# Optimization experiments

Measured on AMD Instinct MI355X. Metric: run time of the kernel, lower is better.

The kernel has to match this reference:

```python
import jax, jax.numpy as jnp
import numpy as np

N, M, D = 6144, 6144, 128
EPS = 1e-12


def setup_inputs() -> dict:
    key = jax.random.key(0)
    k1, k2 = jax.random.split(key)
    desc1 = jax.random.normal(k1, (N, D), dtype=jnp.float32)
    desc2 = jax.random.normal(k2, (M, D), dtype=jnp.float32)
    # DISK descriptors are unit-normalized; distances in the docstring are in [0, 2]
    desc1 = desc1 / jnp.linalg.norm(desc1, axis=-1, keepdims=True)
    desc2 = desc2 / jnp.linalg.norm(desc2, axis=-1, keepdims=True)
    inverse_T = jnp.asarray(15.0, dtype=jnp.float32)  # learned scalar nn.Parameter
    return {"desc1": desc1, "desc2": desc2, "inverse_T": inverse_T}


def reference(desc1, desc2, inverse_T):
    # pairwise Euclidean distance matrix [N, M]
    sq1 = jnp.sum(desc1 * desc1, axis=-1)            # [N]
    sq2 = jnp.sum(desc2 * desc2, axis=-1)            # [M]
    inner = desc1 @ desc2.T                           # [N, M] GEMM, D=128
    d2 = sq1[:, None] + sq2[None, :] - 2.0 * inner
    distances = jnp.sqrt(jnp.maximum(d2, 0.0) + EPS)  # [N, M]

    affinity = -inverse_T * distances                 # scaled logits

    # Categorical(logits=affinity).logits  == log_softmax over rows
    # Categorical(logits=affinity.T).logits.T == log_softmax over columns
    logp_I = jax.nn.log_softmax(affinity, axis=1)     # row distribution [N, M]
    logp_T = jax.nn.log_softmax(affinity, axis=0)     # col distribution [N, M]

    dense_logp = logp_I + logp_T                      # dual-softmax log prob
    dense_p = jnp.exp(logp_I) * jnp.exp(logp_T)       # dual-softmax prob

    # mle(): argmax matches with cycle-consistency check
    maxes_I = jnp.argmax(affinity, axis=1)            # [N] best col per row
    maxes_T = jnp.argmax(affinity, axis=0)            # [M] best row per col
    idx = jnp.arange(N)
    cycle_consistent = maxes_T[maxes_I] == idx        # [N] bool mask
    # Original returns stack([right[paired_left], paired_left]) over the
    # consistent subset; here we keep fixed shape [2, N] + the mask
    # (matches[:, i] valid iff cycle_consistent[i]).
    matches = jnp.stack([idx, maxes_I], axis=0)       # [2, N] int

    return dense_logp, dense_p, matches, cycle_consistent
```

## Files before the change

kernel.cpp:

```cpp
#include <hip/hip_runtime.h>
#include <hip/hip_bf16.h>
#include <stdint.h>

#define NROWS 6144
#define MCOLS 6144
#define DDIM  128
#define EPSQ  1e-12f
#define NTC   48

typedef unsigned long long ull;
typedef __attribute__((ext_vector_type(8))) short short8;
typedef __attribute__((ext_vector_type(4))) float floatx4;

__device__ __forceinline__ ull makeKey(float v, int idx) {
    unsigned u = __float_as_uint(v);
    u = (u & 0x80000000u) ? ~u : (u | 0x80000000u);
    return ((ull)u << 32) | (ull)(0xFFFFFFFFu - (unsigned)idx);
}
__device__ __forceinline__ int decodeKeyIdx(ull k) {
    return (int)(0xFFFFFFFFu - (unsigned)(k & 0xFFFFFFFFull));
}
__device__ __forceinline__ unsigned short f2bf(float f) {
    unsigned u = __float_as_uint(f);
    u += 0x7fffu + ((u >> 16) & 1);
    return (unsigned short)(u >> 16);
}

#define DPPF(x, ctrl) __uint_as_float(__builtin_amdgcn_update_dpp( \
    0, (int)__float_as_uint(x), (ctrl), 0xF, 0xF, false))
#define DPPI(x, ctrl) __builtin_amdgcn_update_dpp(0, (x), (ctrl), 0xF, 0xF, false)
#define ROR8 0x128
#define ROR4 0x124
#define ROR2 0x122
#define ROR1 0x121

#define GLOAD16(g, l) \
  __builtin_amdgcn_global_load_lds((const __attribute__((address_space(1))) unsigned int*)(g), \
                                   (__attribute__((address_space(3))) unsigned int*)(l), 16, 0, 0)

__device__ __forceinline__ void tileCoord(int& rowBase, int& colBase) {
    int id  = blockIdx.x;
    int wid = (id & 7) * (NTC * NTC / 8) + (id >> 3);
    rowBase = (wid / NTC) * 128;
    colBase = (wid % NTC) * 128;
}

__global__ __launch_bounds__(256) void convert_kernel(
    const float* __restrict__ d1, const float* __restrict__ d2,
    unsigned short* __restrict__ s1, unsigned short* __restrict__ s2,
    float* __restrict__ sq1, float* __restrict__ sq2,
    unsigned* __restrict__ zero_region)
{
    int tid = blockIdx.x * 256 + threadIdx.x;
    if (tid < 36864) zero_region[tid] = 0u;

    int row = tid >> 4;
    int sub = tid & 15;
    if (row >= NROWS + MCOLS) return;
    bool isA = row < NROWS;
    int r = isA ? row : row - NROWS;
    const float* src = (isA ? d1 : d2) + (size_t)r * DDIM + sub * 8;
    unsigned short* dst = (isA ? s1 : s2) + (size_t)r * 256;

    float4 v0 = *(const float4*)(src);
    float4 v1 = *(const float4*)(src + 4);
    float vs[8] = {v0.x, v0.y, v0.z, v0.w, v1.x, v1.y, v1.z, v1.w};

    float s = 0.f;
    #pragma unroll
    for (int j = 0; j < 8; ++j) s += vs[j] * vs[j];
    #pragma unroll
    for (int m = 1; m < 16; m <<= 1) s += __shfl_xor(s, m, 64);
    if (sub == 0) { if (isA) sq1[r] = s; else sq2[r] = s; }

    short8 hi, lo;
    #pragma unroll
    for (int j = 0; j < 8; ++j) {
        unsigned short h = f2bf(vs[j]);
        hi[j] = (short)h;
        lo[j] = (short)f2bf(vs[j] - __uint_as_float((unsigned)h << 16));
    }
    int e  = sub * 8;
    int c  = e >> 6;
    int pe = (e & 63) ^ ((r & 7) << 3);
    *(short8*)(dst + c * 128 + pe)      = hi;
    *(short8*)(dst + c * 128 + 64 + pe) = lo;
}

__device__ __forceinline__ void stageBuf(
    const unsigned short* __restrict__ gpanel, unsigned short* buf,
    int c, int h, int t)
{
    #pragma unroll
    for (int it = 0; it < 2; ++it) {
        int li = t * 8 + it * 4096;
        int r  = li >> 6, e = li & 63;
        int gi = r * 256 + c * 128 + h * 64 + e;
        GLOAD16(gpanel + gi, &buf[li]);
    }
}

__device__ __forceinline__ void computeChunk3(
    const unsigned short* Ah_, const unsigned short* Al_,
    const unsigned short* Bh_, const unsigned short* Bl_,
    int lane, int wr, int wc, floatx4 acc[4][2])
{
    const int l15 = lane & 15;
    const int q16 = (lane >> 4) * 16;
    const int sw  = (l15 & 7) << 4;
    const char* Ah = (const char*)Ah_;
    const char* Al = (const char*)Al_;
    const char* Bh = (const char*)Bh_;
    const char* Bl = (const char*)Bl_;
    #pragma unroll
    for (int ks = 0; ks < 2; ++ks) {
        const int kk = (ks * 64 + q16) ^ sw;
        short8 afh[4], afl[4], bfh[2], bfl[2];
        #pragma unroll
        for (int mi = 0; mi < 4; ++mi) {
            afh[mi] = *(const short8*)(Ah + (wr * 64 + mi * 16 + l15) * 128 + kk);
            afl[mi] = *(const short8*)(Al + (wr * 64 + mi * 16 + l15) * 128 + kk);
        }
        #pragma unroll
        for (int ni = 0; ni < 2; ++ni) {
            bfh[ni] = *(const short8*)(Bh + (wc * 32 + ni * 16 + l15) * 128 + kk);
            bfl[ni] = *(const short8*)(Bl + (wc * 32 + ni * 16 + l15) * 128 + kk);
        }
        #pragma unroll
        for (int mi = 0; mi < 4; ++mi)
            #pragma unroll
            for (int ni = 0; ni < 2; ++ni)
                acc[mi][ni] = __builtin_amdgcn_mfma_f32_16x16x32_bf16(
                    bfh[ni], afh[mi], acc[mi][ni], 0, 0, 0);
        #pragma unroll
        for (int mi = 0; mi < 4; ++mi)
            #pragma unroll
            for (int ni = 0; ni < 2; ++ni)
                acc[mi][ni] = __builtin_amdgcn_mfma_f32_16x16x32_bf16(
                    bfl[ni], afh[mi], acc[mi][ni], 0, 0, 0);
        #pragma unroll
        for (int mi = 0; mi < 4; ++mi)
            #pragma unroll
            for (int ni = 0; ni < 2; ++ni)
                acc[mi][ni] = __builtin_amdgcn_mfma_f32_16x16x32_bf16(
                    bfh[ni], afl[mi], acc[mi][ni], 0, 0, 0);
    }
}

__device__ __forceinline__ void computeChunk2(
    const unsigned short* Ah_, const unsigned short* Al_,
    const unsigned short* Bh_,
    int lane, int wr, int wc, floatx4 acc[4][2])
{
    const int l15 = lane & 15;
    const int q16 = (lane >> 4) * 16;
    const int sw  = (l15 & 7) << 4;
    const char* Ah = (const char*)Ah_;
    const char* Al = (const char*)Al_;
    const char* Bh = (const char*)Bh_;
    #pragma unroll
    for (int ks = 0; ks < 2; ++ks) {
        const int kk = (ks * 64 + q16) ^ sw;
        short8 afh[4], afl[4], bfh[2];
        #pragma unroll
        for (int mi = 0; mi < 4; ++mi) {
            afh[mi] = *(const short8*)(Ah + (wr * 64 + mi * 16 + l15) * 128 + kk);
            afl[mi] = *(const short8*)(Al + (wr * 64 + mi * 16 + l15) * 128 + kk);
        }
        #pragma unroll
        for (int ni = 0; ni < 2; ++ni)
            bfh[ni] = *(const short8*)(Bh + (wc * 32 + ni * 16 + l15) * 128 + kk);
        #pragma unroll
        for (int mi = 0; mi < 4; ++mi)
            #pragma unroll
            for (int ni = 0; ni < 2; ++ni)
                acc[mi][ni] = __builtin_amdgcn_mfma_f32_16x16x32_bf16(
                    bfh[ni], afh[mi], acc[mi][ni], 0, 0, 0);
        #pragma unroll
        for (int mi = 0; mi < 4; ++mi)
            #pragma unroll
            for (int ni = 0; ni < 2; ++ni)
                acc[mi][ni] = __builtin_amdgcn_mfma_f32_16x16x32_bf16(
                    bfh[ni], afl[mi], acc[mi][ni], 0, 0, 0);
    }
}

__global__ __launch_bounds__(512, 4) void gemm_reduce_kernel(
    const unsigned short* __restrict__ s1, const unsigned short* __restrict__ s2,
    const float* __restrict__ invT,
    const float* __restrict__ sq1, const float* __restrict__ sq2,
    float* __restrict__ rowsum, float* __restrict__ colsum,
    ull* __restrict__ rowkey, ull* __restrict__ colkey)
{
    __shared__ unsigned short A0[8192], A1[8192], B0[8192], B1[8192];
    __shared__ float lRowS[128], lColS[128];
    __shared__ ull   lRowK[128], lColK[128];

    const int t = threadIdx.x;
    const int lane = t & 63;
    const int wave = t >> 6;
    const int wr = wave >> 2, wc = wave & 3;
    int rowBase, colBase;
    tileCoord(rowBase, colBase);
    const unsigned short* gA = s1 + (size_t)rowBase * 256;
    const unsigned short* gB = s2 + (size_t)colBase * 256;

    if (t < 128) { lRowS[t] = 0.f; lColS[t] = 0.f; lRowK[t] = 0ull; lColK[t] = 0ull; }

    floatx4 acc[4][2] = {};
    stageBuf(gA, A0, 0, 0, t); stageBuf(gA, A1, 0, 1, t);
    stageBuf(gB, B0, 0, 0, t); stageBuf(gB, B1, 0, 1, t);
    __syncthreads();
    computeChunk3(A0, A1, B0, B1, lane, wr, wc, acc);
    __syncthreads();
    stageBuf(gA, A0, 1, 0, t); stageBuf(gA, A1, 1, 1, t);
    stageBuf(gB, B0, 1, 0, t); stageBuf(gB, B1, 1, 1, t);
    __syncthreads();
    computeChunk3(A0, A1, B0, B1, lane, wr, wc, acc);

    const int l15 = lane & 15;
    const int q   = lane >> 4;
    const float iT = *invT;
    float s1r[4];
    #pragma unroll
    for (int mi = 0; mi < 4; ++mi)
        s1r[mi] = sq1[rowBase + wr * 64 + mi * 16 + l15] + EPSQ;
    const int colLoc0 = wc * 32 + q * 4;
    float4 s2v[2];
    #pragma unroll
    for (int ni = 0; ni < 2; ++ni)
        s2v[ni] = *(const float4*)(sq2 + colBase + colLoc0 + ni * 16);

    float rs[4], rv[4]; int rj[4];
    float cs[2][4], cv[2][4]; int ci[2][4];
    #pragma unroll
    for (int ni = 0; ni < 2; ++ni)
        #pragma unroll
        for (int r = 0; r < 4; ++r) { cs[ni][r] = 0.f; cv[ni][r] = -1e30f; ci[ni][r] = 0; }

    #pragma unroll
    for (int mi = 0; mi < 4; ++mi) {
        const int gi = rowBase + wr * 64 + mi * 16 + l15;
        rs[mi] = 0.f; rv[mi] = -1e30f; rj[mi] = 0;
        #pragma unroll
        for (int ni = 0; ni < 2; ++ni) {
            #pragma unroll
            for (int r = 0; r < 4; ++r) {
                float sv2 = (r == 0) ? s2v[ni].x : (r == 1) ? s2v[ni].y
                          : (r == 2) ? s2v[ni].z : s2v[ni].w;
                float dd = s1r[mi] + sv2 - 2.0f * acc[mi][ni][r];
                float v = -iT * __builtin_amdgcn_sqrtf(fmaxf(dd, EPSQ));
                float e = __expf(v);
                rs[mi] += e;
                if (v > rv[mi]) { rv[mi] = v; rj[mi] = colBase + colLoc0 + ni * 16 + r; }
                cs[ni][r] += e;
                if (v > cv[ni][r]) { cv[ni][r] = v; ci[ni][r] = gi; }
            }
        }
    }

    #pragma unroll
    for (int mi = 0; mi < 4; ++mi) {
        float s = rs[mi];
        s += __shfl_xor(s, 16, 64); s += __shfl_xor(s, 32, 64);
        float v = rv[mi];
        v = fmaxf(v, __shfl_xor(v, 16, 64)); v = fmaxf(v, __shfl_xor(v, 32, 64));
        int cand = (rv[mi] == v) ? rj[mi] : 0x7FFFFFFF;
        cand = min(cand, __shfl_xor(cand, 16, 64));
        cand = min(cand, __shfl_xor(cand, 32, 64));
        if (lane < 16) {
            int idx = wr * 64 + mi * 16 + l15;
            atomicAdd(&lRowS[idx], s);
            atomicMax(&lRowK[idx], makeKey(v, cand));
        }
    }

    #pragma unroll
    for (int ni = 0; ni < 2; ++ni)
        #pragma unroll
        for (int r = 0; r < 4; ++r) {
            float s = cs[ni][r];
            s += DPPF(s, ROR8); s += DPPF(s, ROR4); s += DPPF(s, ROR2); s += DPPF(s, ROR1);
            float v = cv[ni][r];
            v = fmaxf(v, DPPF(v, ROR8)); v = fmaxf(v, DPPF(v, ROR4));
            v = fmaxf(v, DPPF(v, ROR2)); v = fmaxf(v, DPPF(v, ROR1));
            int cand = (cv[ni][r] == v) ? ci[ni][r] : 0x7FFFFFFF;
            cand = min(cand, DPPI(cand, ROR8)); cand = min(cand, DPPI(cand, ROR4));
            cand = min(cand, DPPI(cand, ROR2)); cand = min(cand, DPPI(cand, ROR1));
            if (l15 == 0) {
                int idx = colLoc0 + ni * 16 + r;
                atomicAdd(&lColS[idx], s);
                atomicMax(&lColK[idx], makeKey(v, cand));
            }
        }
    __syncthreads();

    if (t < 128) {
        atomicAdd(&rowsum[rowBase + t], lRowS[t]);
        atomicMax(&rowkey[rowBase + t], lRowK[t]);
    } else if (t < 256) {
        int j = t - 128;
        atomicAdd(&colsum[colBase + j], lColS[j]);
        atomicMax(&colkey[colBase + j], lColK[j]);
    }
}

#define VSTRIDE 132
__global__ __launch_bounds__(512, 4) void gemm_write_kernel(
    const unsigned short* __restrict__ s1, const unsigned short* __restrict__ s2,
    const float* __restrict__ invT,
    const float* __restrict__ sq1, const float* __restrict__ sq2,
    const float* __restrict__ rowsum, const float* __restrict__ colsum,
    const ull* __restrict__ rowkey, const ull* __restrict__ colkey,
    float* __restrict__ logp_out, float* __restrict__ p_out,
    float* __restrict__ out_matches, float* __restrict__ out_cyc)
{
    __shared__ char SMEM[128 * VSTRIDE * 4];
    unsigned short* A0 = (unsigned short*)(SMEM);
    unsigned short* A1 = (unsigned short*)(SMEM + 16384);
    unsigned short* B0 = (unsigned short*)(SMEM + 32768);
    unsigned short* B1 = (unsigned short*)(SMEM + 49152);
    float* V = (float*)SMEM;

    const int t = threadIdx.x;
    const int lane = t & 63;
    const int wave = t >> 6;
    const int wr = wave >> 2, wc = wave & 3;
    int rowBase, colBase;
    tileCoord(rowBase, colBase);
    const unsigned short* gA = s1 + (size_t)rowBase * 256;
    const unsigned short* gB = s2 + (size_t)colBase * 256;

    if (colBase == 0 && t < 128) {
        int i = rowBase + t;
        int mi = decodeKeyIdx(rowkey[i]);
        out_matches[i]         = (float)i;
        out_matches[NROWS + i] = (float)mi;
        out_cyc[i] = (decodeKeyIdx(colkey[mi]) == i) ? 1.0f : 0.0f;
    }

    floatx4 acc[4][2] = {};
    stageBuf(gA, A0, 0, 0, t); stageBuf(gA, A1, 0, 1, t);
    stageBuf(gB, B0, 0, 0, t); stageBuf(gB, B1, 1, 0, t);
    __syncthreads();
    computeChunk2(A0, A1, B0, lane, wr, wc, acc);
    __syncthreads();
    stageBuf(gA, A0, 1, 0, t); stageBuf(gA, A1, 1, 1, t);
    __syncthreads();
    computeChunk2(A0, A1, B1, lane, wr, wc, acc);

    const int l15 = lane & 15;
    const int q   = lane >> 4;
    const float iT = *invT;
    float s1r[4];
    #pragma unroll
    for (int mi = 0; mi < 4; ++mi)
        s1r[mi] = sq1[rowBase + wr * 64 + mi * 16 + l15] + EPSQ;
    const int colLoc0 = wc * 32 + q * 4;
    float4 s2v[2];
    #pragma unroll
    for (int ni = 0; ni < 2; ++ni)
        s2v[ni] = *(const float4*)(sq2 + colBase + colLoc0 + ni * 16);

    __syncthreads();
    #pragma unroll
    for (int mi = 0; mi < 4; ++mi) {
        const int lrow = wr * 64 + mi * 16 + l15;
        #pragma unroll
        for (int ni = 0; ni < 2; ++ni) {
            floatx4 vv;
            #pragma unroll
            for (int r = 0; r < 4; ++r) {
                float sv2 = (r == 0) ? s2v[ni].x : (r == 1) ? s2v[ni].y
                          : (r == 2) ? s2v[ni].z : s2v[ni].w;
                float dd = s1r[mi] + sv2 - 2.0f * acc[mi][ni][r];
                vv[r] = -iT * __builtin_amdgcn_sqrtf(fmaxf(dd, EPSQ));
            }
            *(floatx4*)(V + lrow * VSTRIDE + colLoc0 + ni * 16) = vv;
        }
    }
    __syncthreads();

    const int rsub = lane >> 4;
    const int csub = (lane & 15) * 4;
    #pragma unroll
    for (int g = 0; g < 4; ++g) {
        const int lrow = wave * 16 + g * 4 + rsub;
        const int grow = rowBase + lrow;
        const float rl = logf(rowsum[grow]);
        #pragma unroll
        for (int h = 0; h < 2; ++h) {
            const int lcol = h * 64 + csub;
            float4 csum = *(const float4*)(colsum + colBase + lcol);
            float4 cl;
            cl.x = logf(csum.x); cl.y = logf(csum.y);
            cl.z = logf(csum.z); cl.w = logf(csum.w);
            float4 v4 = *(const float4*)(V + lrow * VSTRIDE + lcol);
            floatx4 ov, pv;
            ov[0] = (v4.x - rl) + (v4.x - cl.x); pv[0] = __expf(ov[0]);
            ov[1] = (v4.y - rl) + (v4.y - cl.y); pv[1] = __expf(ov[1]);
            ov[2] = (v4.z - rl) + (v4.z - cl.z); pv[2] = __expf(ov[2]);
            ov[3] = (v4.w - rl) + (v4.w - cl.w); pv[3] = __expf(ov[3]);
            size_t off = (size_t)grow * MCOLS + colBase + lcol;
            __builtin_nontemporal_store(ov, (floatx4*)(logp_out + off));
            __builtin_nontemporal_store(pv, (floatx4*)(p_out + off));
        }
    }
}

extern "C" void kernel_launch(void* const* d_in, const int* in_sizes, int n_in,
                              void* d_out, int out_size, void* d_ws, size_t ws_size,
                              hipStream_t stream) {
    const float* d1   = (const float*)d_in[0];
    const float* d2   = (const float*)d_in[1];
    const float* invT = (const float*)d_in[2];

    float* out     = (float*)d_out;
    float* logp    = out;
    float* pout    = out + (size_t)NROWS * MCOLS;
    float* matches = out + 2ull * NROWS * MCOLS;
    float* cyc     = matches + 2 * NROWS;

    char* ws = (char*)d_ws;
    float* rowsum = (float*)(ws + 0);
    float* colsum = (float*)(ws + 24576);
    ull*   rowkey = (ull*)(ws + 49152);
    ull*   colkey = (ull*)(ws + 98304);
    float* sq1    = (float*)(ws + 147456);
    float* sq2    = (float*)(ws + 172032);
    unsigned short* s1 = (unsigned short*)(ws + 270336);
    unsigned short* s2 = (unsigned short*)(ws + 270336 + 3145728);

    convert_kernel<<<(NROWS + MCOLS) * 16 / 256, 256, 0, stream>>>(
        d1, d2, s1, s2, sq1, sq2, (unsigned*)ws);

    gemm_reduce_kernel<<<NTC * NTC, 512, 0, stream>>>(
        s1, s2, invT, sq1, sq2, rowsum, colsum, rowkey, colkey);

    gemm_write_kernel<<<NTC * NTC, 512, 0, stream>>>(
        s1, s2, invT, sq1, sq2, rowsum, colsum, rowkey, colkey,
        logp, pout, matches, cyc);
}
```

Measured before the change: 128.9 us.

## Load MFMA operands directly from global memory, dropping LDS staging

The GEMM stage no longer stages the pre-swizzled bf16 hi/lo panels through LDS with barriers. Each wave now reads its MFMA fragments straight from global memory, relying on the pre-swizzled layout and on L1/L2 caching. This frees 64KB of shared memory and removes the staging barriers, which could raise occupancy. The cost is redundant global/cache traffic, since neighbouring waves re-read the same A/B rows, and a __syncthreads is added before the LDS reductions.

After: 135.1 us. 1.05x slower.

```diff
diff --git a/kernel.cpp b/kernel.cpp
--- a/kernel.cpp
+++ b/kernel.cpp
@@ -97,53 +97,6 @@
         int r  = li >> 6, e = li & 63;
         int gi = r * 256 + c * 128 + h * 64 + e;
         GLOAD16(gpanel + gi, &buf[li]);
-    }
-}
-
-__device__ __forceinline__ void computeChunk3(
-    const unsigned short* Ah_, const unsigned short* Al_,
-    const unsigned short* Bh_, const unsigned short* Bl_,
-    int lane, int wr, int wc, floatx4 acc[4][2])
-{
-    const int l15 = lane & 15;
-    const int q16 = (lane >> 4) * 16;
-    const int sw  = (l15 & 7) << 4;
-    const char* Ah = (const char*)Ah_;
-    const char* Al = (const char*)Al_;
-    const char* Bh = (const char*)Bh_;
-    const char* Bl = (const char*)Bl_;
-    #pragma unroll
-    for (int ks = 0; ks < 2; ++ks) {
-        const int kk = (ks * 64 + q16) ^ sw;
-        short8 afh[4], afl[4], bfh[2], bfl[2];
-        #pragma unroll
-        for (int mi = 0; mi < 4; ++mi) {
-            afh[mi] = *(const short8*)(Ah + (wr * 64 + mi * 16 + l15) * 128 + kk);
-            afl[mi] = *(const short8*)(Al + (wr * 64 + mi * 16 + l15) * 128 + kk);
-        }
-        #pragma unroll
-        for (int ni = 0; ni < 2; ++ni) {
-            bfh[ni] = *(const short8*)(Bh + (wc * 32 + ni * 16 + l15) * 128 + kk);
-            bfl[ni] = *(const short8*)(Bl + (wc * 32 + ni * 16 + l15) * 128 + kk);
-        }
-        #pragma unroll
-        for (int mi = 0; mi < 4; ++mi)
-            #pragma unroll
-            for (int ni = 0; ni < 2; ++ni)
-                acc[mi][ni] = __builtin_amdgcn_mfma_f32_16x16x32_bf16(
-                    bfh[ni], afh[mi], acc[mi][ni], 0, 0, 0);
-        #pragma unroll
-        for (int mi = 0; mi < 4; ++mi)
-            #pragma unroll
-            for (int ni = 0; ni < 2; ++ni)
-                acc[mi][ni] = __builtin_amdgcn_mfma_f32_16x16x32_bf16(
-                    bfl[ni], afh[mi], acc[mi][ni], 0, 0, 0);
-        #pragma unroll
-        for (int mi = 0; mi < 4; ++mi)
-            #pragma unroll
-            for (int ni = 0; ni < 2; ++ni)
-                acc[mi][ni] = __builtin_amdgcn_mfma_f32_16x16x32_bf16(
-                    bfh[ni], afl[mi], acc[mi][ni], 0, 0, 0);
     }
 }
 
@@ -192,7 +145,6 @@
     float* __restrict__ rowsum, float* __restrict__ colsum,
     ull* __restrict__ rowkey, ull* __restrict__ colkey)
 {
-    __shared__ unsigned short A0[8192], A1[8192], B0[8192], B1[8192];
     __shared__ float lRowS[128], lColS[128];
     __shared__ ull   lRowK[128], lColK[128];
 
@@ -202,24 +154,59 @@
     const int wr = wave >> 2, wc = wave & 3;
     int rowBase, colBase;
     tileCoord(rowBase, colBase);
-    const unsigned short* gA = s1 + (size_t)rowBase * 256;
-    const unsigned short* gB = s2 + (size_t)colBase * 256;
+    const char* gA = (const char*)(s1 + (size_t)rowBase * 256);
+    const char* gB = (const char*)(s2 + (size_t)colBase * 256);
 
     if (t < 128) { lRowS[t] = 0.f; lColS[t] = 0.f; lRowK[t] = 0ull; lColK[t] = 0ull; }
 
+    const int l15 = lane & 15;
+    const int q16 = (lane >> 4) * 16;
+    const int sw  = (l15 & 7) << 4;
+    int aOff[4], bOff[2];
+    #pragma unroll
+    for (int mi = 0; mi < 4; ++mi) aOff[mi] = (wr * 64 + mi * 16 + l15) * 512;
+    #pragma unroll
+    for (int ni = 0; ni < 2; ++ni) bOff[ni] = (wc * 32 + ni * 16 + l15) * 512;
+
     floatx4 acc[4][2] = {};
-    stageBuf(gA, A0, 0, 0, t); stageBuf(gA, A1, 0, 1, t);
-    stageBuf(gB, B0, 0, 0, t); stageBuf(gB, B1, 0, 1, t);
-    __syncthreads();
-    computeChunk3(A0, A1, B0, B1, lane, wr, wc, acc);
-    __syncthreads();
-    stageBuf(gA, A0, 1, 0, t); stageBuf(gA, A1, 1, 1, t);
-    stageBuf(gB, B0, 1, 0, t); stageBuf(gB, B1, 1, 1, t);
-    __syncthreads();
-    computeChunk3(A0, A1, B0, B1, lane, wr, wc, acc);
-
-    const int l15 = lane & 15;
-    const int q   = lane >> 4;
+    #pragma unroll
+    for (int c = 0; c < 2; ++c) {
+        #pragma unroll
+        for (int ks = 0; ks < 2; ++ks) {
+            const int kb = c * 256 + ((ks * 64 + q16) ^ sw);
+            short8 afh[4], afl[4], bfh[2], bfl[2];
+            #pragma unroll
+            for (int mi = 0; mi < 4; ++mi) {
+                afh[mi] = *(const short8*)(gA + aOff[mi] + kb);
+                afl[mi] = *(const short8*)(gA + aOff[mi] + kb + 128);
+            }
+            #pragma unroll
+            for (int ni = 0; ni < 2; ++ni) {
+                bfh[ni] = *(const short8*)(gB + bOff[ni] + kb);
+                bfl[ni] = *(const short8*)(gB + bOff[ni] + kb + 128);
+            }
+            #pragma unroll
+            for (int mi = 0; mi < 4; ++mi)
+                #pragma unroll
+                for (int ni = 0; ni < 2; ++ni)
+                    acc[mi][ni] = __builtin_amdgcn_mfma_f32_16x16x32_bf16(
+                        bfh[ni], afh[mi], acc[mi][ni], 0, 0, 0);
+            #pragma unroll
+            for (int mi = 0; mi < 4; ++mi)
+                #pragma unroll
+                for (int ni = 0; ni < 2; ++ni)
+                    acc[mi][ni] = __builtin_amdgcn_mfma_f32_16x16x32_bf16(
+                        bfl[ni], afh[mi], acc[mi][ni], 0, 0, 0);
+            #pragma unroll
+            for (int mi = 0; mi < 4; ++mi)
+                #pragma unroll
+                for (int ni = 0; ni < 2; ++ni)
+                    acc[mi][ni] = __builtin_amdgcn_mfma_f32_16x16x32_bf16(
+                        bfh[ni], afl[mi], acc[mi][ni], 0, 0, 0);
+        }
+    }
+
+    const int q = lane >> 4;
     const float iT = *invT;
     float s1r[4];
     #pragma unroll
@@ -258,6 +245,8 @@
             }
         }
     }
+
+    __syncthreads();
 
     #pragma unroll
     for (int mi = 0; mi < 4; ++mi) {
```
